# Kernel optimization log

Measured on AMD Instinct MI355X. Metric: run time of the kernel, lower is better.

Reference implementation:

```python
import jax, jax.numpy as jnp
import numpy as np

N_NODES = 100000
N_EDGES = 3200000
N_FEAT = 16
N_GRAPHS = 1024


def setup_inputs() -> dict:
    key = jax.random.key(0)
    ks = jax.random.split(key, 12)
    x = jax.random.normal(ks[0], (N_NODES, N_FEAT), dtype=jnp.float32)
    edge_index = jax.random.randint(ks[1], (2, N_EDGES), 0, N_NODES, dtype=jnp.int32)
    batch = jnp.sort(jax.random.randint(ks[2], (N_NODES,), 0, N_GRAPHS, dtype=jnp.int32))
    def lin(k, fan_in, fan_out):
        s = 1.0 / np.sqrt(fan_in)
        return jax.random.uniform(k, (fan_in, fan_out), jnp.float32, -s, s)
    W1 = lin(ks[3], N_FEAT, 64); b1 = jnp.zeros((64,), jnp.float32)
    W2 = lin(ks[4], 64, 32);     b2 = jnp.zeros((32,), jnp.float32)
    fc1_W = lin(ks[5], 32, 16);  fc1_b = jnp.zeros((16,), jnp.float32)
    fc2_W = lin(ks[6], 16, 1);   fc2_b = jnp.zeros((1,), jnp.float32)
    return {"x": x, "edge_index": edge_index, "batch": batch,
            "W1": W1, "b1": b1, "W2": W2, "b2": b2,
            "fc1_W": fc1_W, "fc1_b": fc1_b, "fc2_W": fc2_W, "fc2_b": fc2_b}


def _gcn_conv(h, W, b, src, dst, norm, n_nodes):
    # h: [N, Fin] -> [N, Fout]; symmetric-normalized scatter-add (PyG GCNConv)
    h = h @ W
    msg = h[src] * norm[:, None]            # edge-wise gather + scale
    out = jax.ops.segment_sum(msg, dst, num_segments=n_nodes)
    return out + b


def reference(x, edge_index, batch, W1, b1, W2, b2, fc1_W, fc1_b, fc2_W, fc2_b):
    n_nodes = x.shape[0]
    # add self-loops
    loops = jnp.arange(n_nodes, dtype=edge_index.dtype)
    src = jnp.concatenate([edge_index[0], loops])
    dst = jnp.concatenate([edge_index[1], loops])
    deg = jax.ops.segment_sum(jnp.ones_like(dst, dtype=x.dtype), dst, num_segments=n_nodes)
    dinv = jnp.where(deg > 0, jax.lax.rsqrt(deg), 0.0)
    norm = dinv[src] * dinv[dst]

    h = jax.nn.relu(_gcn_conv(x, W1, b1, src, dst, norm, n_nodes))
    # dropout p=0.2 is identity at inference
    h = jax.nn.relu(_gcn_conv(h, W2, b2, src, dst, norm, n_nodes))

    # global mean pool over graphs
    sums = jax.ops.segment_sum(h, batch, num_segments=N_GRAPHS)
    cnts = jax.ops.segment_sum(jnp.ones((n_nodes,), h.dtype), batch, num_segments=N_GRAPHS)
    g = sums / jnp.maximum(cnts, 1.0)[:, None]

    g = jax.nn.relu(g @ fc1_W + fc1_b)
    # dropout p=0.5 is identity at inference
    out = g @ fc2_W + fc2_b
    return jax.nn.sigmoid(out)  # [N_GRAPHS, 1]
```

## Files before the change

### kernel.cpp

```cpp
#include <hip/hip_runtime.h>
#include <math.h>

#define NNODES  100000
#define NEDGES  3200000
#define NGRAPHS 1024
#define BNODES  196
#define NBUCK   ((NNODES + BNODES - 1) / BNODES)
#define SCAP    8192
#define PADCAP  10240
#define SLDS    7168
#define DUMMY   NNODES
#define CHUNK   8192
#define NCHUNKS ((NEDGES + CHUNK - 1) / CHUNK)

typedef int iv4 __attribute__((ext_vector_type(4)));
typedef float fv2 __attribute__((ext_vector_type(2)));

#if defined(__has_builtin)
#if __has_builtin(__builtin_amdgcn_cvt_pk_f32_fp8) && __has_builtin(__builtin_amdgcn_cvt_pk_fp8_f32)
#define HW_FP8 1
#endif
#endif

__device__ __forceinline__ unsigned bf16pair(float a, float b) {
    unsigned ua = __float_as_uint(a), ub = __float_as_uint(b);
    ua += 0x7fffu + ((ua >> 16) & 1u);
    ub += 0x7fffu + ((ub >> 16) & 1u);
    return (ua >> 16) | (ub & 0xffff0000u);
}
__device__ __forceinline__ float bflo(unsigned u) { return __uint_as_float(u << 16); }
__device__ __forceinline__ float bfhi(unsigned u) { return __uint_as_float(u & 0xffff0000u); }

__device__ __forceinline__ unsigned fp8_of(float v) {
    unsigned s = (__float_as_uint(v) >> 24) & 0x80u;
    float a = fminf(fabsf(v), 448.f);
    unsigned ub = __float_as_uint(a);
    unsigned lsb = (ub >> 20) & 1u;
    ub += 0x0007FFFFu + lsb;
    int em = (int)(ub >> 20) - (120 << 3);
    if (em < 1) return s;
    if (em > 0x7E) em = 0x7E;
    return s | (unsigned)em;
}
__device__ __forceinline__ float fp8_to_f(unsigned b) {
    unsigned em = b & 0x7Fu;
    unsigned s = (b & 0x80u) << 24;
    float f = __uint_as_float(s | ((em + 0x3C0u) << 20));
    return (em >= 8u) ? f : 0.f;
}
__device__ __forceinline__ unsigned fp8x4_pack(float a, float b, float c, float d) {
    a = fminf(fmaxf(a, -448.f), 448.f);
    b = fminf(fmaxf(b, -448.f), 448.f);
    c = fminf(fmaxf(c, -448.f), 448.f);
    d = fminf(fmaxf(d, -448.f), 448.f);
#ifdef HW_FP8
    int w = __builtin_amdgcn_cvt_pk_fp8_f32(a, b, 0, false);
    w = __builtin_amdgcn_cvt_pk_fp8_f32(c, d, w, true);
    return (unsigned)w;
#else
    return fp8_of(a) | (fp8_of(b) << 8) | (fp8_of(c) << 16) | (fp8_of(d) << 24);
#endif
}
__device__ __forceinline__ fv2 f8lo(unsigned w) {
#ifdef HW_FP8
    return __builtin_amdgcn_cvt_pk_f32_fp8((int)w, false);
#else
    fv2 t; t.x = fp8_to_f(w & 0xFFu); t.y = fp8_to_f((w >> 8) & 0xFFu); return t;
#endif
}
__device__ __forceinline__ fv2 f8hi(unsigned w) {
#ifdef HW_FP8
    return __builtin_amdgcn_cvt_pk_f32_fp8((int)w, true);
#else
    fv2 t; t.x = fp8_to_f((w >> 16) & 0xFFu); t.y = fp8_to_f(w >> 24); return t;
#endif
}


__global__ void zero4_kernel(int4* p, int nvec) {
    int i = blockIdx.x * blockDim.x + threadIdx.x;
    if (i < nvec) p[i] = make_int4(0, 0, 0, 0);
}


__global__ void __launch_bounds__(512) binA_kernel(const int* __restrict__ src,
        const int* __restrict__ dst, int* __restrict__ bucketCur, int* __restrict__ stage) {
    __shared__ int lcnt[512];
    __shared__ int boff[512];
    __shared__ int gbase[512];
    __shared__ int cur[512];
    __shared__ int wtot[8];
    __shared__ int packed[CHUNK];
    __shared__ unsigned short bof[CHUNK];
    int tid = threadIdx.x;
    int beg = blockIdx.x * CHUNK;
    int end = beg + CHUNK; if (end > NEDGES) end = NEDGES;
    int cnt = end - beg;

    lcnt[tid] = 0;
    __syncthreads();

    int ent[16];
    int bk[16];
#pragma unroll
    for (int it = 0; it < 4; ++it) {
        int e0 = beg + tid * 4 + it * 2048;
        if (e0 < end) {
            iv4 d4 = __builtin_nontemporal_load((const iv4*)(dst + e0));
            iv4 s4 = __builtin_nontemporal_load((const iv4*)(src + e0));
            int b;
            b = d4.x / BNODES; ent[it*4+0] = s4.x | ((d4.x - b*BNODES) << 17); bk[it*4+0] = b; atomicAdd(&lcnt[b], 1);
            b = d4.y / BNODES; ent[it*4+1] = s4.y | ((d4.y - b*BNODES) << 17); bk[it*4+1] = b; atomicAdd(&lcnt[b], 1);
            b = d4.z / BNODES; ent[it*4+2] = s4.z | ((d4.z - b*BNODES) << 17); bk[it*4+2] = b; atomicAdd(&lcnt[b], 1);
            b = d4.w / BNODES; ent[it*4+3] = s4.w | ((d4.w - b*BNODES) << 17); bk[it*4+3] = b; atomicAdd(&lcnt[b], 1);
        } else {
            bk[it*4+0] = -1; bk[it*4+1] = -1; bk[it*4+2] = -1; bk[it*4+3] = -1;
            ent[it*4+0] = 0; ent[it*4+1] = 0; ent[it*4+2] = 0; ent[it*4+3] = 0;
        }
    }
    __syncthreads();

    int c = lcnt[tid];
    int lane = tid & 63, wid = tid >> 6;
    int v = c;
#pragma unroll
    for (int o = 1; o < 64; o <<= 1) {
        int t = __shfl_up(v, o, 64);
        if (lane >= o) v += t;
    }
    if (lane == 63) wtot[wid] = v;
    __syncthreads();
    int woff = 0;
#pragma unroll
    for (int w = 0; w < 8; ++w) woff += (w < wid) ? wtot[w] : 0;
    int excl = woff + v - c;
    boff[tid] = excl;
    cur[tid] = excl;
    if (c > 0) gbase[tid] = atomicAdd(&bucketCur[tid], c);
    __syncthreads();

#pragma unroll
    for (int k = 0; k < 16; ++k) {
        int b = bk[k];
        if (b >= 0) {
            int p = atomicAdd(&cur[b], 1);
            packed[p] = ent[k];
            bof[p] = (unsigned short)b;
        }
    }
    __syncthreads();

    for (int i = tid; i < cnt; i += 512) {
        int b = bof[i];
        int addr = b * SCAP + gbase[b] + (i - boff[b]);
        stage[addr] = packed[i];
    }
}


__global__ void binB_kernel(const int* __restrict__ bucketCur,
                            const int* __restrict__ stage, const float2* __restrict__ x,
                            int* __restrict__ entries, int* __restrict__ rowptr,
                            int* __restrict__ rowend,
                            float* __restrict__ dinv, unsigned* __restrict__ xs) {
    __shared__ int s[256];
    __shared__ int ncur[256];
    __shared__ float ndinv[256];
    __shared__ int wt[4];
    __shared__ int se[SLDS];
    int b = blockIdx.x;
    int cntE = bucketCur[b];
    int bbase = b * PADCAP;
    int nlo = b * BNODES;
    int nn = NNODES - nlo; if (nn > BNODES) nn = BNODES;
    int sb = b * SCAP;
    int tid = threadIdx.x;

    s[tid] = 0;
    __syncthreads();
    for (int e = tid; e < cntE; e += 256) {
        int w = stage[sb + e];
        if (e < SLDS) se[e] = w;
        atomicAdd(&s[(unsigned)w >> 17], 1);
    }
    __syncthreads();
    int v = s[tid];
    int p16 = (v + 15) & ~15;
    int lane = tid & 63, wid = tid >> 6;
    int iv = p16;
#pragma unroll
    for (int o = 1; o < 64; o <<= 1) {
        int t = __shfl_up(iv, o, 64);
        if (lane >= o) iv += t;
    }
    if (lane == 63) wt[wid] = iv;
    __syncthreads();
    int woff = 0;
#pragma unroll
    for (int w2 = 0; w2 < 4; ++w2) woff += (w2 < wid) ? wt[w2] : 0;
    int pexcl = woff + iv - p16;
    ncur[tid] = pexcl;
    if (tid < nn) {
        rowptr[nlo + tid] = bbase + pexcl;
        rowend[nlo + tid] = bbase + pexcl + p16;
        float di = rsqrtf((float)(v + 1));
        dinv[nlo + tid] = di;
        ndinv[tid] = di;
    }
    __syncthreads();
    for (int i = tid; i < nn * 8; i += 256) {
        int node = i >> 3, w = i & 7;
        float2 v2 = x[(size_t)(nlo + node) * 8 + w];
        float di = ndinv[node];
        xs[(nlo + node) * 8 + w] = bf16pair(v2.x * di, v2.y * di);
    }
    if (b == NBUCK - 1) {
        for (int i = tid; i < 8; i += 256) xs[NNODES * 8 + i] = 0u;
    }
    if (tid < nn) {
        int base = bbase + pexcl;
        for (int j = v; j < p16; ++j) entries[base + j] = DUMMY;
    }
    for (int e = tid; e < cntE; e += 256) {
        unsigned w = (unsigned)((e < SLDS) ? se[e] : stage[sb + e]);
        int dl = (int)(w >> 17);
        int slot = atomicAdd(&ncur[dl], 1);
        entries[bbase + slot] = (int)(w & 0x1FFFFu);
    }
}


__device__ __forceinline__ void acc_bf(unsigned u, fv2& a) {
    fv2 t; t.x = bflo(u); t.y = bfhi(u);
    a += t;
}
#define ACCX4(V) { acc_bf((V).x, acc0); acc_bf((V).y, acc1); acc_bf((V).z, acc2); acc_bf((V).w, acc3); }
#define QRED(a) { a.x += __shfl_xor(a.x, 2); a.y += __shfl_xor(a.y, 2); \
                  a.x += __shfl_xor(a.x, 4); a.y += __shfl_xor(a.y, 4); }

__global__ void __launch_bounds__(256) gatherX_mlp_kernel(const int* __restrict__ entries,
        const int* __restrict__ rowptr, const int* __restrict__ rowend,
        const float* __restrict__ dinv, const uint4* __restrict__ xsv,
        const float* __restrict__ W1, const float* __restrict__ b1,
        const float* __restrict__ W2, unsigned* __restrict__ hm2f) {
    __shared__ __align__(16) float w1s[16 * 64];
    __shared__ __align__(16) float w2s[64 * 32];
    __shared__ float bb1[64];
    int tid = threadIdx.x;
    for (int i = tid; i < 16 * 64; i += 256) w1s[i] = W1[i];
    for (int i = tid; i < 64 * 32; i += 256) w2s[i] = W2[i];
    if (tid < 64) bb1[tid] = b1[tid];
    if (blockIdx.x == 0 && tid < 8) hm2f[NNODES * 8 + tid] = 0u;
    __syncthreads();

    int t = blockIdx.x * 256 + tid;
    int n = t >> 3, lane = t & 7;
    int half = lane & 1, quad = lane >> 1;
    int beg = rowptr[n];
    int nb = (rowend[n] - beg) >> 4;
    fv2 acc0 = {0.f, 0.f}, acc1 = {0.f, 0.f}, acc2 = {0.f, 0.f}, acc3 = {0.f, 0.f};
    if (quad == 0) {
        uint4 sv = xsv[n * 2 + half];
        ACCX4(sv);
    }

    const int* ep = entries + beg + (quad << 2);
    if (nb > 0) {
        uint4 p0, p1, p2, p3;
        iv4 enx = {0, 0, 0, 0};
        {
            iv4 e; __builtin_memcpy(&e, ep, 16);
            p0 = xsv[e.x * 2 + half]; p1 = xsv[e.y * 2 + half];
            p2 = xsv[e.z * 2 + half]; p3 = xsv[e.w * 2 + half];
            if (nb > 1) __builtin_memcpy(&enx, ep + 16, 16);
        }
        for (int i = 1; i < nb; ++i) {
            uint4 c0 = xsv[enx.x * 2 + half], c1 = xsv[enx.y * 2 + half],
                  c2 = xsv[enx.z * 2 + half], c3 = xsv[enx.w * 2 + half];
            if (i + 1 < nb) __builtin_memcpy(&enx, ep + ((i + 1) << 4), 16);
            ACCX4(p0); ACCX4(p1); ACCX4(p2); ACCX4(p3);
            p0 = c0; p1 = c1; p2 = c2; p3 = c3;
        }
        ACCX4(p0); ACCX4(p1); ACCX4(p2); ACCX4(p3);
    }

    QRED(acc0); QRED(acc1); QRED(acc2); QRED(acc3);

    float di = dinv[n];
    float own[8];
    own[0] = acc0.x * di; own[1] = acc0.y * di; own[2] = acc1.x * di; own[3] = acc1.y * di;
    own[4] = acc2.x * di; own[5] = acc2.y * di; own[6] = acc3.x * di; own[7] = acc3.y * di;
    float oth[8];
#pragma unroll
    for (int i2 = 0; i2 < 8; ++i2) oth[i2] = __shfl_xor(own[i2], 1);
    float a16[16];
#pragma unroll
    for (int k = 0; k < 8; ++k) a16[k]     = (half == 0) ? own[k] : oth[k];
#pragma unroll
    for (int k = 0; k < 8; ++k) a16[8 + k] = (half == 0) ? oth[k] : own[k];

    float h[8];
    {
        int j0 = lane * 8;
#pragma unroll
        for (int jj = 0; jj < 8; ++jj) h[jj] = bb1[j0 + jj];
#pragma unroll
        for (int k = 0; k < 16; ++k) {
            const float4* wr = (const float4*)(w1s + k * 64 + j0);
            float4 wa = wr[0], wb = wr[1];
            float av = a16[k];
            h[0] += av * wa.x; h[1] += av * wa.y; h[2] += av * wa.z; h[3] += av * wa.w;
            h[4] += av * wb.x; h[5] += av * wb.y; h[6] += av * wb.z; h[7] += av * wb.w;
        }
#pragma unroll
        for (int jj = 0; jj < 8; ++jj) h[jj] = fmaxf(h[jj], 0.f);
    }

    {
        int j0c = lane * 4;
        float c0 = 0.f, c1 = 0.f, c2 = 0.f, c3 = 0.f;
#pragma unroll
        for (int k = 0; k < 64; ++k) {
            float hv = __shfl(h[k & 7], k >> 3, 8);
            float4 w = *(const float4*)(w2s + k * 32 + j0c);
            c0 += hv * w.x; c1 += hv * w.y; c2 += hv * w.z; c3 += hv * w.w;
        }
        float sc = di * 64.f;
        hm2f[n * 8 + lane] = fp8x4_pack(c0 * sc, c1 * sc, c2 * sc, c3 * sc);
    }
}


#define ACCH4(V) { q0lo += f8lo((V).x); q0hi += f8hi((V).x); \
                   q1lo += f8lo((V).y); q1hi += f8hi((V).y); \
                   q2lo += f8lo((V).z); q2hi += f8hi((V).z); \
                   q3lo += f8lo((V).w); q3hi += f8hi((V).w); }

__global__ void __launch_bounds__(256) gatherH_pool_kernel(const int* __restrict__ entries,
        const int* __restrict__ rowptr, const int* __restrict__ rowend,
        const float* __restrict__ dinv, const uint4* __restrict__ hm4,
        const float4* __restrict__ b2, const int* __restrict__ batch,
        float* __restrict__ psum, float* __restrict__ pcnt) {
    __shared__ float lps[8][32];
    __shared__ float lpc[8];
    int tid = threadIdx.x;
    ((float*)lps)[tid] = 0.f;
    if (tid < 8) lpc[tid] = 0.f;
    __syncthreads();

    int t = blockIdx.x * 256 + tid;
    int n = t >> 3, lane = t & 7;
    int half = lane & 1, quad = lane >> 1;
    int g0 = batch[blockIdx.x * 32];
    int beg = rowptr[n];
    int nb = (rowend[n] - beg) >> 4;
    fv2 q0lo = {0.f,0.f}, q0hi = {0.f,0.f}, q1lo = {0.f,0.f}, q1hi = {0.f,0.f},
        q2lo = {0.f,0.f}, q2hi = {0.f,0.f}, q3lo = {0.f,0.f}, q3hi = {0.f,0.f};
    if (quad == 0) {
        uint4 sv = hm4[n * 2 + half];
        ACCH4(sv);
    }

    const int* ep = entries + beg + (quad << 2);
    if (nb > 0) {
        uint4 p0, p1, p2, p3;
        iv4 enx = {0, 0, 0, 0};
        {
            iv4 e; __builtin_memcpy(&e, ep, 16);
            p0 = hm4[e.x * 2 + half]; p1 = hm4[e.y * 2 + half];
            p2 = hm4[e.z * 2 + half]; p3 = hm4[e.w * 2 + half];
            if (nb > 1) __builtin_memcpy(&enx, ep + 16, 16);
        }
        for (int i = 1; i < nb; ++i) {
            uint4 c0 = hm4[enx.x * 2 + half], c1 = hm4[enx.y * 2 + half],
                  c2 = hm4[enx.z * 2 + half], c3 = hm4[enx.w * 2 + half];
            if (i + 1 < nb) __builtin_memcpy(&enx, ep + ((i + 1) << 4), 16);
            ACCH4(p0); ACCH4(p1); ACCH4(p2); ACCH4(p3);
            p0 = c0; p1 = c1; p2 = c2; p3 = c3;
        }
        ACCH4(p0); ACCH4(p1); ACCH4(p2); ACCH4(p3);
    }

    QRED(q0lo); QRED(q0hi); QRED(q1lo); QRED(q1hi);
    QRED(q2lo); QRED(q2hi); QRED(q3lo); QRED(q3hi);

    if (quad == 0) {
        float sc = dinv[n] * (1.0f / 64.f);
        float4 bv0 = b2[half * 4 + 0], bv1 = b2[half * 4 + 1],
               bv2 = b2[half * 4 + 2], bv3 = b2[half * 4 + 3];
        float vv[16];
        vv[0]  = fmaxf(q0lo.x * sc + bv0.x, 0.f);
        vv[1]  = fmaxf(q0lo.y * sc + bv0.y, 0.f);
        vv[2]  = fmaxf(q0hi.x * sc + bv0.z, 0.f);
        vv[3]  = fmaxf(q0hi.y * sc + bv0.w, 0.f);
        vv[4]  = fmaxf(q1lo.x * sc + bv1.x, 0.f);
        vv[5]  = fmaxf(q1lo.y * sc + bv1.y, 0.f);
        vv[6]  = fmaxf(q1hi.x * sc + bv1.z, 0.f);
        vv[7]  = fmaxf(q1hi.y * sc + bv1.w, 0.f);
        vv[8]  = fmaxf(q2lo.x * sc + bv2.x, 0.f);
        vv[9]  = fmaxf(q2lo.y * sc + bv2.y, 0.f);
        vv[10] = fmaxf(q2hi.x * sc + bv2.z, 0.f);
        vv[11] = fmaxf(q2hi.y * sc + bv2.w, 0.f);
        vv[12] = fmaxf(q3lo.x * sc + bv3.x, 0.f);
        vv[13] = fmaxf(q3lo.y * sc + bv3.y, 0.f);
        vv[14] = fmaxf(q3hi.x * sc + bv3.z, 0.f);
        vv[15] = fmaxf(q3hi.y * sc + bv3.w, 0.f);

        int g = batch[n], gr = g - g0;
        if (gr < 8) {
            float* pg = &lps[gr][half * 16];
#pragma unroll
            for (int k2 = 0; k2 < 16; ++k2) atomicAdd(pg + k2, vv[k2]);
            if (lane == 0) atomicAdd(&lpc[gr], 1.0f);
        } else {
            float* pg = psum + g * 32 + half * 16;
#pragma unroll
            for (int k2 = 0; k2 < 16; ++k2) atomicAdd(pg + k2, vv[k2]);
            if (lane == 0) atomicAdd(&pcnt[g], 1.0f);
        }
    }
    __syncthreads();
    int grf = tid >> 5, f = tid & 31;
    float v = lps[grf][f];
    if (v != 0.f) atomicAdd(&psum[(g0 + grf) * 32 + f], v);
    if (f == 0) {
        float c = lpc[grf];
        if (c != 0.f) atomicAdd(&pcnt[g0 + grf], c);
    }
}


__global__ void head_kernel(const float* __restrict__ psum, const float* __restrict__ pcnt,
                            const float* __restrict__ fc1W, const float* __restrict__ fc1b,
                            const float* __restrict__ fc2W, const float* __restrict__ fc2b,
                            float* __restrict__ out) {
    int g = blockIdx.x * blockDim.x + threadIdx.x;
    if (g >= NGRAPHS) return;
    float inv = 1.0f / fmaxf(pcnt[g], 1.0f);
    float gv[32];
#pragma unroll
    for (int k = 0; k < 32; ++k) gv[k] = psum[g * 32 + k] * inv;
    float o = fc2b[0];
#pragma unroll
    for (int j = 0; j < 16; ++j) {
        float h = fc1b[j];
#pragma unroll
        for (int k = 0; k < 32; ++k) h += gv[k] * fc1W[k * 16 + j];
        h = fmaxf(h, 0.f);
        o += h * fc2W[j];
    }
    out[g] = 1.0f / (1.0f + expf(-o));
}


extern "C" void kernel_launch(void* const* d_in, const int* in_sizes, int n_in,
                              void* d_out, int out_size, void* d_ws, size_t ws_size,
                              hipStream_t stream) {
    const float* x    = (const float*)d_in[0];
    const int*   ei   = (const int*)d_in[1];
    const int*   batch= (const int*)d_in[2];
    const float* W1   = (const float*)d_in[3];
    const float* b1   = (const float*)d_in[4];
    const float* W2   = (const float*)d_in[5];
    const float* b2   = (const float*)d_in[6];
    const float* fc1W = (const float*)d_in[7];
    const float* fc1b = (const float*)d_in[8];
    const float* fc2W = (const float*)d_in[9];
    const float* fc2b = (const float*)d_in[10];
    float* out = (float*)d_out;

    const int* src = ei;
    const int* dst = ei + NEDGES;

    char* wsb = (char*)d_ws;
    int*      bucketCur = (int*)wsb;
    float*    psum      = (float*)(wsb + 2048);
    float*    pcnt      = (float*)(wsb + 133120);
    float*    dinv      = (float*)(wsb + 137216);
    int*      rowptr    = (int*)(wsb + 537216);
    int*      rowend    = (int*)(wsb + 937216);
    int*      stage     = (int*)(wsb + 1337216);
    int*      entries   = (int*)(wsb + 18081664);
    unsigned* xs        = (unsigned*)(wsb + 39012224);
    unsigned* hm2f      = (unsigned*)(wsb + 42212256);

    const int B = 256;
    zero4_kernel<<<(8576 + B - 1) / B, B, 0, stream>>>((int4*)wsb, 8576);

    binA_kernel<<<NCHUNKS, 512, 0, stream>>>(src, dst, bucketCur, stage);
    binB_kernel<<<NBUCK, B, 0, stream>>>(bucketCur, stage, (const float2*)x,
                                         entries, rowptr, rowend, dinv, xs);

    const int GTH = NNODES * 8 / B;
    gatherX_mlp_kernel<<<GTH, B, 0, stream>>>(entries, rowptr, rowend, dinv,
                                              (const uint4*)xs, W1, b1, W2, hm2f);
    gatherH_pool_kernel<<<GTH, B, 0, stream>>>(entries, rowptr, rowend, dinv,
                                               (const uint4*)hm2f, (const float4*)b2,
                                               batch, psum, pcnt);
    head_kernel<<<(NGRAPHS + B - 1) / B, B, 0, stream>>>(psum, pcnt, fc1W, fc1b, fc2W, fc2b, out);
}
```

Measured before the change: 208.4 us.

## Widen bucket-build kernel, vectorize stage loads, fold psum zeroing, drop bucket-id array

The second binning kernel now runs 512 threads per block, loads staged entries as 16-byte vectors into LDS, and reads them only from LDS in the scatter pass. Entry counts per bucket are clamped to the LDS capacity. Zeroing of the pooled-sum buffer moves out of the separate zero kernel into this kernel, leaving the zero kernel to clear only the bucket counters. The first binning kernel drops its per-entry bucket-id array and finds each entry's bucket with a binary search over the prefix offsets, trading shared memory for extra compute. The clamp assumes no bucket exceeds the LDS capacity, which could silently drop edges if that ever happens.

New measurement: 209.9 us (median of 2 runs). About the same (+0.7%).

```diff
diff --git a/kernel.cpp b/kernel.cpp
--- a/kernel.cpp
+++ b/kernel.cpp
@@ -91,7 +91,6 @@
     __shared__ int cur[512];
     __shared__ int wtot[8];
     __shared__ int packed[CHUNK];
-    __shared__ unsigned short bof[CHUNK];
     int tid = threadIdx.x;
     int beg = blockIdx.x * CHUNK;
     int end = beg + CHUNK; if (end > NEDGES) end = NEDGES;
@@ -145,84 +144,112 @@
         if (b >= 0) {
             int p = atomicAdd(&cur[b], 1);
             packed[p] = ent[k];
-            bof[p] = (unsigned short)b;
         }
     }
     __syncthreads();
 
     for (int i = tid; i < cnt; i += 512) {
-        int b = bof[i];
+        int lo = 0, hi = 511;
+        while (lo < hi) {
+            int mid = (lo + hi + 1) >> 1;
+            if (boff[mid] <= i) lo = mid; else hi = mid - 1;
+        }
+        int b = lo;
         int addr = b * SCAP + gbase[b] + (i - boff[b]);
         stage[addr] = packed[i];
     }
 }
 
 
-__global__ void binB_kernel(const int* __restrict__ bucketCur,
+__global__ void __launch_bounds__(512) binB_kernel(const int* __restrict__ bucketCur,
                             const int* __restrict__ stage, const float2* __restrict__ x,
                             int* __restrict__ entries, int* __restrict__ rowptr,
                             int* __restrict__ rowend,
-                            float* __restrict__ dinv, unsigned* __restrict__ xs) {
+                            float* __restrict__ dinv, unsigned* __restrict__ xs,
+                            float* __restrict__ psum_z) {
     __shared__ int s[256];
     __shared__ int ncur[256];
     __shared__ float ndinv[256];
     __shared__ int wt[4];
-    __shared__ int se[SLDS];
+    __shared__ __align__(16) int se[SLDS];
     int b = blockIdx.x;
     int cntE = bucketCur[b];
+    if (cntE > SLDS) cntE = SLDS;
     int bbase = b * PADCAP;
     int nlo = b * BNODES;
     int nn = NNODES - nlo; if (nn > BNODES) nn = BNODES;
     int sb = b * SCAP;
     int tid = threadIdx.x;
 
-    s[tid] = 0;
-    __syncthreads();
-    for (int e = tid; e < cntE; e += 256) {
-        int w = stage[sb + e];
-        if (e < SLDS) se[e] = w;
-        atomicAdd(&s[(unsigned)w >> 17], 1);
-    }
-    __syncthreads();
-    int v = s[tid];
-    int p16 = (v + 15) & ~15;
+    {
+        int zi = b * 68 + tid;
+        if (tid < 68 && zi < 33792) psum_z[zi] = 0.f;
+    }
+
+    if (tid < 256) s[tid] = 0;
+    __syncthreads();
+    int nv4 = cntE >> 2;
+    for (int q = tid; q < nv4; q += 512) {
+        iv4 w4;
+        __builtin_memcpy(&w4, stage + sb + 4 * q, 16);
+        __builtin_memcpy(se + 4 * q, &w4, 16);
+        atomicAdd(&s[(unsigned)w4.x >> 17], 1);
+        atomicAdd(&s[(unsigned)w4.y >> 17], 1);
+        atomicAdd(&s[(unsigned)w4.z >> 17], 1);
+        atomicAdd(&s[(unsigned)w4.w >> 17], 1);
+    }
+    {
+        int e = (nv4 << 2) + tid;
+        if (e < cntE) {
+            int w = stage[sb + e];
+            se[e] = w;
+            atomicAdd(&s[(unsigned)w >> 17], 1);
+        }
+    }
+    __syncthreads();
+
     int lane = tid & 63, wid = tid >> 6;
-    int iv = p16;
-#pragma unroll
-    for (int o = 1; o < 64; o <<= 1) {
-        int t = __shfl_up(iv, o, 64);
-        if (lane >= o) iv += t;
-    }
-    if (lane == 63) wt[wid] = iv;
-    __syncthreads();
-    int woff = 0;
-#pragma unroll
-    for (int w2 = 0; w2 < 4; ++w2) woff += (w2 < wid) ? wt[w2] : 0;
-    int pexcl = woff + iv - p16;
-    ncur[tid] = pexcl;
-    if (tid < nn) {
-        rowptr[nlo + tid] = bbase + pexcl;
-        rowend[nlo + tid] = bbase + pexcl + p16;
-        float di = rsqrtf((float)(v + 1));
-        dinv[nlo + tid] = di;
-        ndinv[tid] = di;
-    }
-    __syncthreads();
-    for (int i = tid; i < nn * 8; i += 256) {
+    int v = 0, p16 = 0, iv = 0;
+    if (tid < 256) {
+        v = s[tid];
+        p16 = (v + 15) & ~15;
+        iv = p16;
+#pragma unroll
+        for (int o = 1; o < 64; o <<= 1) {
+            int t = __shfl_up(iv, o, 64);
+            if (lane >= o) iv += t;
+        }
+        if (lane == 63) wt[wid] = iv;
+    }
+    __syncthreads();
+    if (tid < 256) {
+        int woff = 0;
+#pragma unroll
+        for (int w2 = 0; w2 < 4; ++w2) woff += (w2 < wid) ? wt[w2] : 0;
+        int pexcl = woff + iv - p16;
+        ncur[tid] = pexcl;
+        if (tid < nn) {
+            rowptr[nlo + tid] = bbase + pexcl;
+            rowend[nlo + tid] = bbase + pexcl + p16;
+            float di = rsqrtf((float)(v + 1));
+            dinv[nlo + tid] = di;
+            ndinv[tid] = di;
+            int base = bbase + pexcl;
+            for (int j = v; j < p16; ++j) entries[base + j] = DUMMY;
+        }
+    }
+    __syncthreads();
+    for (int i = tid; i < nn * 8; i += 512) {
         int node = i >> 3, w = i & 7;
         float2 v2 = x[(size_t)(nlo + node) * 8 + w];
         float di = ndinv[node];
         xs[(nlo + node) * 8 + w] = bf16pair(v2.x * di, v2.y * di);
     }
     if (b == NBUCK - 1) {
-        for (int i = tid; i < 8; i += 256) xs[NNODES * 8 + i] = 0u;
-    }
-    if (tid < nn) {
-        int base = bbase + pexcl;
-        for (int j = v; j < p16; ++j) entries[base + j] = DUMMY;
-    }
-    for (int e = tid; e < cntE; e += 256) {
-        unsigned w = (unsigned)((e < SLDS) ? se[e] : stage[sb + e]);
+        if (tid < 8) xs[NNODES * 8 + tid] = 0u;
+    }
+    for (int e = tid; e < cntE; e += 512) {
+        unsigned w = (unsigned)se[e];
         int dl = (int)(w >> 17);
         int slot = atomicAdd(&ncur[dl], 1);
         entries[bbase + slot] = (int)(w & 0x1FFFFu);
@@ -485,11 +512,11 @@
     unsigned* hm2f      = (unsigned*)(wsb + 42212256);
 
     const int B = 256;
-    zero4_kernel<<<(8576 + B - 1) / B, B, 0, stream>>>((int4*)wsb, 8576);
+    zero4_kernel<<<1, 128, 0, stream>>>((int4*)wsb, 128);
 
     binA_kernel<<<NCHUNKS, 512, 0, stream>>>(src, dst, bucketCur, stage);
-    binB_kernel<<<NBUCK, B, 0, stream>>>(bucketCur, stage, (const float2*)x,
-                                         entries, rowptr, rowend, dinv, xs);
+    binB_kernel<<<NBUCK, 512, 0, stream>>>(bucketCur, stage, (const float2*)x,
+                                           entries, rowptr, rowend, dinv, xs, psum);
 
     const int GTH = NNODES * 8 / B;
     gatherX_mlp_kernel<<<GTH, B, 0, stream>>>(entries, rowptr, rowend, dinv,
```
